# Kernel tuning notes

Measured on AMD Instinct MI355X. Metric: run time of the kernel, lower is better.

## Reference

```python
import jax, jax.numpy as jnp
import numpy as np

TEMPERATURE = 0.07
EPS = 1e-12  # F.normalize eps


def _construct_labels(visual_ids, anchor_idx):
    # Faithful vectorization of the original order-dependent double loop:
    # for i < B-1: final write to labels[i] comes from pair (i, B-1)
    #   -> 1 iff ids[i]==anchor_id and ids[B-1]==anchor_id, else 0
    # for i == B-1: final write comes from pair (B-2, B-1)
    #   -> 1 iff ids[B-1]==anchor_id and ids[B-2]==anchor_id, else 0
    B = visual_ids.shape[0]
    anchor_id = visual_ids[anchor_idx]
    same = visual_ids == anchor_id  # [B] bool
    labels = jnp.where(same & same[B - 1], 1, 0).astype(jnp.int32)
    labels = labels.at[B - 1].set((same[B - 1] & same[B - 2]).astype(jnp.int32))
    return labels


def setup_inputs() -> dict:
    key = jax.random.key(0)
    k1, k2 = jax.random.split(key)
    visual_feat = jax.random.normal(k1, (8192, 512), dtype=jnp.float32)
    visual_ids = jax.random.randint(k2, (8192,), 0, 1024, dtype=jnp.int64 if jax.config.jax_enable_x64 else jnp.int32)
    anchor_idx = 3
    return {"visual_feat": visual_feat, "visual_ids": visual_ids, "anchor_idx": anchor_idx}


def reference(visual_feat, visual_ids, anchor_idx):
    # L2 normalize rows (F.normalize: x / max(||x||, eps))
    norm = jnp.sqrt(jnp.sum(visual_feat * visual_feat, axis=1, keepdims=True))
    f = visual_feat / jnp.maximum(norm, EPS)
    sim = jnp.matmul(f, f.T) / TEMPERATURE  # [B, B]
    labels = _construct_labels(visual_ids, anchor_idx)  # [B] int in {0,1}
    logp = jax.nn.log_softmax(sim, axis=-1)  # [B, B]
    picked = jnp.take_along_axis(logp, labels[:, None], axis=1)[:, 0]
    loss = -jnp.mean(picked)
    return loss
```

## Files before the change

### kernel.cpp

```cpp
#include <hip/hip_runtime.h>


typedef int i32x8 __attribute__((ext_vector_type(8)));
typedef float f32x4 __attribute__((ext_vector_type(4)));

#define B_N 8192
#define D_K 512
#define ROWB 512
#define INVT 14.285714285714286f
#define SCALE_LOG2 20.609929155556622f

static __device__ __forceinline__ void load16_to_lds(const void* g, void* l) {
  __builtin_amdgcn_global_load_lds(
      (const __attribute__((address_space(1))) unsigned int*)g,
      (__attribute__((address_space(3))) unsigned int*)l, 16, 0, 0);
}

__global__ __launch_bounds__(256)
void norm_kernel(const float* __restrict__ x,
                 unsigned char* __restrict__ fQ,
                 float* __restrict__ Z) {
  const int row = blockIdx.x * 4 + (threadIdx.x >> 6);
  const int lane = threadIdx.x & 63;
  const float4* xr = (const float4*)(x + (size_t)row * D_K);
  float4 a = xr[2 * lane];
  float4 b = xr[2 * lane + 1];
  float s = a.x * a.x + a.y * a.y + a.z * a.z + a.w * a.w +
            b.x * b.x + b.y * b.y + b.z * b.z + b.w * b.w;
#pragma unroll
  for (int off = 1; off < 64; off <<= 1) s += __shfl_xor(s, off);
  const float inv = 1.0f / fmaxf(sqrtf(s), 1e-12f);
  int lo = 0, hi = 0;
  lo = __builtin_amdgcn_cvt_pk_fp8_f32(a.x * inv, a.y * inv, lo, false);
  lo = __builtin_amdgcn_cvt_pk_fp8_f32(a.z * inv, a.w * inv, lo, true);
  hi = __builtin_amdgcn_cvt_pk_fp8_f32(b.x * inv, b.y * inv, hi, false);
  hi = __builtin_amdgcn_cvt_pk_fp8_f32(b.z * inv, b.w * inv, hi, true);
  int2 p; p.x = lo; p.y = hi;
  ((int2*)(fQ + (size_t)row * ROWB))[lane] = p;
  if (lane == 0) Z[row] = 0.0f;
}

__global__ __launch_bounds__(256, 2)
void sim_kernel(const unsigned char* __restrict__ fQ,
                float* __restrict__ Z, float* __restrict__ T01,
                float* __restrict__ D) {
  __shared__ unsigned char ldsA[128 * 128];
  __shared__ unsigned char ldsB[128 * 128];

  const int tid = threadIdx.x;
  const int lane = tid & 63;
  const int w = tid >> 6;
  const int wm = w & 1;
  const int wn = w >> 1;
  const int I0 = blockIdx.x * 128;
  const int Jbase = blockIdx.y * 1024;

  const int srow = lane >> 3;
  const int sg = (lane & 7) ^ srow;
  const size_t sOff = (size_t)srow * ROWB + sg * 16;

  const int fr = lane & 15;
  const int q = lane >> 4;
  const int swz = fr & 7;

  const unsigned char* raBase = ldsA + (wm * 64 + fr) * 128;
  const unsigned char* rbBase = ldsB + (wn * 64 + fr) * 128;
  const int off0 = ((2 * q) ^ swz) * 16;
  const int off1 = ((2 * q + 1) ^ swz) * 16;

  float Zp[4][4];
#pragma unroll
  for (int m = 0; m < 4; ++m)
#pragma unroll
    for (int r = 0; r < 4; ++r) Zp[m][r] = 0.0f;

#pragma unroll 1
  for (int jt = 0; jt < 8; ++jt) {
    const int J0 = Jbase + jt * 128;
    f32x4 acc[4][4];
#pragma unroll
    for (int m = 0; m < 4; ++m)
#pragma unroll
      for (int n = 0; n < 4; ++n) acc[m][n] = (f32x4){0.f, 0.f, 0.f, 0.f};

#pragma unroll 1
    for (int kk = 0; kk < 4; ++kk) {
      const int k0 = kk * 128;
      {
        const unsigned char* gA = fQ + (size_t)(I0 + w * 32) * ROWB + k0 + sOff;
        unsigned char* lA = ldsA + (w * 32) * 128;
#pragma unroll
        for (int rr = 0; rr < 32; rr += 8)
          load16_to_lds(gA + (size_t)rr * ROWB, lA + rr * 128);
      }
      {
        const unsigned char* gB = fQ + (size_t)(J0 + w * 32) * ROWB + k0 + sOff;
        unsigned char* lB = ldsB + (w * 32) * 128;
#pragma unroll
        for (int rr = 0; rr < 32; rr += 8)
          load16_to_lds(gB + (size_t)rr * ROWB, lB + rr * 128);
      }
      __syncthreads();

      i32x8 bv[4];
#pragma unroll
      for (int n = 0; n < 4; ++n) {
        const unsigned char* rb = rbBase + n * 16 * 128;
        int4 r0 = *(const int4*)(rb + off0);
        int4 r1 = *(const int4*)(rb + off1);
        bv[n] = (i32x8){r0.x, r0.y, r0.z, r0.w, r1.x, r1.y, r1.z, r1.w};
      }
#pragma unroll
      for (int mh = 0; mh < 2; ++mh) {
        i32x8 av[2];
#pragma unroll
        for (int m = 0; m < 2; ++m) {
          const unsigned char* ra = raBase + (mh * 2 + m) * 16 * 128;
          int4 r0 = *(const int4*)(ra + off0);
          int4 r1 = *(const int4*)(ra + off1);
          av[m] = (i32x8){r0.x, r0.y, r0.z, r0.w, r1.x, r1.y, r1.z, r1.w};
        }
#pragma unroll
        for (int m = 0; m < 2; ++m)
#pragma unroll
          for (int n = 0; n < 4; ++n)
            acc[mh * 2 + m][n] = __builtin_amdgcn_mfma_scale_f32_16x16x128_f8f6f4(
                av[m], bv[n], acc[mh * 2 + m][n], 0, 0, 0, 127, 0, 127);
      }
      __syncthreads();
    }

    if (blockIdx.y == 0 && jt == 0 && wn == 0 && fr < 2) {
#pragma unroll
      for (int m = 0; m < 4; ++m)
#pragma unroll
        for (int r = 0; r < 4; ++r) {
          const int row = I0 + wm * 64 + m * 16 + q * 4 + r;
          T01[row * 2 + fr] = acc[m][0][r] * INVT;
        }
    }

    if (blockIdx.y == (blockIdx.x >> 3) && jt == (blockIdx.x & 7)) {
#pragma unroll
      for (int m = 0; m < 4; ++m)
#pragma unroll
        for (int n = 0; n < 4; ++n) {
          const int col = J0 + wn * 64 + n * 16 + fr;
#pragma unroll
          for (int r = 0; r < 4; ++r) {
            const int row = I0 + wm * 64 + m * 16 + q * 4 + r;
            if (row == col) D[row] = acc[m][n][r];
          }
        }
    }

#pragma unroll
    for (int m = 0; m < 4; ++m)
#pragma unroll
      for (int n = 0; n < 4; ++n)
#pragma unroll
        for (int r = 0; r < 4; ++r)
          Zp[m][r] += exp2f((acc[m][n][r] - 1.0f) * SCALE_LOG2);
  }

#pragma unroll
  for (int m = 0; m < 4; ++m)
#pragma unroll
    for (int r = 0; r < 4; ++r) {
      float v = Zp[m][r];
      v += __shfl_xor(v, 1);
      v += __shfl_xor(v, 2);
      v += __shfl_xor(v, 4);
      v += __shfl_xor(v, 8);
      if (fr == 0) atomicAdd(&Z[I0 + wm * 64 + m * 16 + q * 4 + r], v);
    }
}

__global__ __launch_bounds__(1024)
void finalize_kernel(const float* __restrict__ Z,
                     const float* __restrict__ T01,
                     const float* __restrict__ D,
                     const int* __restrict__ ids,
                     const int* __restrict__ anchor,
                     float* __restrict__ out) {
  __shared__ float red[1024];
  const int t = threadIdx.x;
  const int anchor_id = ids[anchor[0]];
  const int sameLast = (ids[B_N - 1] == anchor_id);
  const int samePrev = (ids[B_N - 2] == anchor_id);
  float sum = 0.0f;
#pragma unroll
  for (int it = 0; it < B_N / 1024; ++it) {
    const int i = it * 1024 + t;
    const int same_i = (ids[i] == anchor_id);
    const int lab = (i < B_N - 1) ? (same_i & sameLast) : (sameLast & samePrev);
    const float tt = T01[i * 2 + lab];
    const float Zc = Z[i] - exp2f((D[i] - 1.0f) * SCALE_LOG2) + 1.0f;
    sum += tt - (INVT + logf(Zc));
  }
  red[t] = sum;
  __syncthreads();
  for (int off = 512; off > 0; off >>= 1) {
    if (t < off) red[t] += red[t + off];
    __syncthreads();
  }
  if (t == 0) out[0] = -red[0] / (float)B_N;
}

extern "C" void kernel_launch(void* const* d_in, const int* in_sizes, int n_in,
                              void* d_out, int out_size, void* d_ws, size_t ws_size,
                              hipStream_t stream) {
  const float* x = (const float*)d_in[0];
  const int* ids = (const int*)d_in[1];
  const int* anchor = (const int*)d_in[2];
  float* out = (float*)d_out;

  unsigned char* fQ = (unsigned char*)d_ws;
  float* Z = (float*)((char*)d_ws + (size_t)B_N * ROWB);
  float* T01 = Z + B_N;
  float* D = T01 + 2 * B_N;

  norm_kernel<<<B_N / 4, 256, 0, stream>>>(x, fQ, Z);
  sim_kernel<<<dim3(64, 8), 256, 0, stream>>>(fQ, Z, T01, D);
  finalize_kernel<<<1, 1024, 0, stream>>>(Z, T01, D, ids, anchor, out);
}
```

Measured before the change: 122.7 us.

## Fuse finalize reduction into sim kernel via last-block atomic counter

Removes the separate finalize kernel launch. Each sim block increments a global counter when it finishes, and the last block to arrive computes the log-softmax loss reduction. Stores to T01 and D become agent-scope atomics so the last block sees them after a threadfence. Launch bounds also change to allow 3 blocks per CU. The cost is a serialized tail: one 256-thread block does all the final work.

```diff
diff --git a/kernel.cpp b/kernel.cpp
--- a/kernel.cpp
+++ b/kernel.cpp
@@ -7,8 +7,12 @@
 #define B_N 8192
 #define D_K 512
 #define ROWB 512
+#define NBLK 512
 #define INVT 14.285714285714286f
 #define SCALE_LOG2 20.609929155556622f
+
+#define AGENT_LOAD(p) __hip_atomic_load((p), __ATOMIC_RELAXED, __HIP_MEMORY_SCOPE_AGENT)
+#define AGENT_STORE(p, v) __hip_atomic_store((p), (v), __ATOMIC_RELAXED, __HIP_MEMORY_SCOPE_AGENT)
 
 static __device__ __forceinline__ void load16_to_lds(const void* g, void* l) {
   __builtin_amdgcn_global_load_lds(
@@ -19,7 +23,8 @@
 __global__ __launch_bounds__(256)
 void norm_kernel(const float* __restrict__ x,
                  unsigned char* __restrict__ fQ,
-                 float* __restrict__ Z) {
+                 float* __restrict__ Z,
+                 unsigned int* __restrict__ cnt) {
   const int row = blockIdx.x * 4 + (threadIdx.x >> 6);
   const int lane = threadIdx.x & 63;
   const float4* xr = (const float4*)(x + (size_t)row * D_K);
@@ -38,22 +43,29 @@
   int2 p; p.x = lo; p.y = hi;
   ((int2*)(fQ + (size_t)row * ROWB))[lane] = p;
   if (lane == 0) Z[row] = 0.0f;
-}
-
-__global__ __launch_bounds__(256, 2)
+  if (blockIdx.x == 0 && threadIdx.x == 0) cnt[0] = 0u;
+}
+
+__global__ __launch_bounds__(256, 3)
 void sim_kernel(const unsigned char* __restrict__ fQ,
                 float* __restrict__ Z, float* __restrict__ T01,
-                float* __restrict__ D) {
+                float* __restrict__ D,
+                const int* __restrict__ ids,
+                const int* __restrict__ anchor,
+                unsigned int* __restrict__ cnt,
+                float* __restrict__ out) {
   __shared__ unsigned char ldsA[128 * 128];
   __shared__ unsigned char ldsB[128 * 128];
+  __shared__ unsigned int s_last;
 
   const int tid = threadIdx.x;
   const int lane = tid & 63;
   const int w = tid >> 6;
   const int wm = w & 1;
   const int wn = w >> 1;
-  const int I0 = blockIdx.x * 128;
-  const int Jbase = blockIdx.y * 1024;
+  const int bx = blockIdx.x, by = blockIdx.y;
+  const int I0 = bx * 128;
+  const int Jbase = by * 1024;
 
   const int srow = lane >> 3;
   const int sg = (lane & 7) ^ srow;
@@ -130,17 +142,17 @@
       __syncthreads();
     }
 
-    if (blockIdx.y == 0 && jt == 0 && wn == 0 && fr < 2) {
+    if (by == 0 && jt == 0 && wn == 0 && fr < 2) {
 #pragma unroll
       for (int m = 0; m < 4; ++m)
 #pragma unroll
         for (int r = 0; r < 4; ++r) {
           const int row = I0 + wm * 64 + m * 16 + q * 4 + r;
-          T01[row * 2 + fr] = acc[m][0][r] * INVT;
+          AGENT_STORE(&T01[row * 2 + fr], acc[m][0][r] * INVT);
         }
     }
 
-    if (blockIdx.y == (blockIdx.x >> 3) && jt == (blockIdx.x & 7)) {
+    if (by == (bx >> 3) && jt == (bx & 7)) {
 #pragma unroll
       for (int m = 0; m < 4; ++m)
 #pragma unroll
@@ -149,7 +161,7 @@
 #pragma unroll
           for (int r = 0; r < 4; ++r) {
             const int row = I0 + wm * 64 + m * 16 + q * 4 + r;
-            if (row == col) D[row] = acc[m][n][r];
+            if (row == col) AGENT_STORE(&D[row], acc[m][n][r]);
           }
         }
     }
@@ -174,37 +186,50 @@
       v += __shfl_xor(v, 8);
       if (fr == 0) atomicAdd(&Z[I0 + wm * 64 + m * 16 + q * 4 + r], v);
     }
-}
-
-__global__ __launch_bounds__(1024)
-void finalize_kernel(const float* __restrict__ Z,
-                     const float* __restrict__ T01,
-                     const float* __restrict__ D,
-                     const int* __restrict__ ids,
-                     const int* __restrict__ anchor,
-                     float* __restrict__ out) {
-  __shared__ float red[1024];
-  const int t = threadIdx.x;
+
+  __syncthreads();
+  __threadfence();
+  if (tid == 0) s_last = atomicAdd(cnt, 1u);
+  __syncthreads();
+  if (s_last != NBLK - 1) return;
+  __threadfence();
+
   const int anchor_id = ids[anchor[0]];
   const int sameLast = (ids[B_N - 1] == anchor_id);
   const int samePrev = (ids[B_N - 2] == anchor_id);
   float sum = 0.0f;
-#pragma unroll
-  for (int it = 0; it < B_N / 1024; ++it) {
-    const int i = it * 1024 + t;
-    const int same_i = (ids[i] == anchor_id);
-    const int lab = (i < B_N - 1) ? (same_i & sameLast) : (sameLast & samePrev);
-    const float tt = T01[i * 2 + lab];
-    const float Zc = Z[i] - exp2f((D[i] - 1.0f) * SCALE_LOG2) + 1.0f;
-    sum += tt - (INVT + logf(Zc));
+#pragma unroll 1
+  for (int ib = 0; ib < 8; ++ib) {
+    int i[4];
+    float z[4], d[4], t0[4], t1[4];
+    int id[4];
+#pragma unroll
+    for (int u = 0; u < 4; ++u) {
+      i[u] = (ib * 4 + u) * 256 + tid;
+      z[u] = AGENT_LOAD(&Z[i[u]]);
+      d[u] = AGENT_LOAD(&D[i[u]]);
+      t0[u] = AGENT_LOAD(&T01[i[u] * 2 + 0]);
+      t1[u] = AGENT_LOAD(&T01[i[u] * 2 + 1]);
+      id[u] = ids[i[u]];
+    }
+#pragma unroll
+    for (int u = 0; u < 4; ++u) {
+      const int same_i = (id[u] == anchor_id);
+      const int lab =
+          (i[u] < B_N - 1) ? (same_i & sameLast) : (sameLast & samePrev);
+      const float tt = lab ? t1[u] : t0[u];
+      const float Zc = z[u] - exp2f((d[u] - 1.0f) * SCALE_LOG2) + 1.0f;
+      sum += tt - (INVT + logf(Zc));
+    }
   }
-  red[t] = sum;
+  float* red = (float*)ldsA;
+  red[tid] = sum;
   __syncthreads();
-  for (int off = 512; off > 0; off >>= 1) {
-    if (t < off) red[t] += red[t + off];
+  for (int off = 128; off > 0; off >>= 1) {
+    if (tid < off) red[tid] += red[tid + off];
     __syncthreads();
   }
-  if (t == 0) out[0] = -red[0] / (float)B_N;
+  if (tid == 0) out[0] = -red[0] / (float)B_N;
 }
 
 extern "C" void kernel_launch(void* const* d_in, const int* in_sizes, int n_in,
@@ -219,8 +244,8 @@
   float* Z = (float*)((char*)d_ws + (size_t)B_N * ROWB);
   float* T01 = Z + B_N;
   float* D = T01 + 2 * B_N;
-
-  norm_kernel<<<B_N / 4, 256, 0, stream>>>(x, fQ, Z);
-  sim_kernel<<<dim3(64, 8), 256, 0, stream>>>(fQ, Z, T01, D);
-  finalize_kernel<<<1, 1024, 0, stream>>>(Z, T01, D, ids, anchor, out);
-}
+  unsigned int* cnt = (unsigned int*)(D + B_N);
+
+  norm_kernel<<<B_N / 4, 256, 0, stream>>>(x, fQ, Z, cnt);
+  sim_kernel<<<dim3(64, 8), 256, 0, stream>>>(fQ, Z, T01, D, ids, anchor, cnt, out);
+}
```

New measurement: 158.9 us. +29.5%, slower.

## Keep the full A row panel resident in LDS across all column tiles

Applied to the files above, without the earlier changes.

The sim kernel now loads the block's 128x512 fp8 A panel into LDS once, across four k-slices, instead of reloading it for every column tile. Only the B tile is streamed in the inner loop, roughly halving per-iteration global-to-LDS traffic. The LDS swizzle and the read offsets are changed to a new k-chunk permutation. The finalize kernel now issues all of its loads up front. The cost is LDS use rising to about 80KB per block, which may limit occupancy.

```diff
diff --git a/kernel.cpp b/kernel.cpp
--- a/kernel.cpp
+++ b/kernel.cpp
@@ -44,7 +44,7 @@
 void sim_kernel(const unsigned char* __restrict__ fQ,
                 float* __restrict__ Z, float* __restrict__ T01,
                 float* __restrict__ D) {
-  __shared__ unsigned char ldsA[128 * 128];
+  __shared__ unsigned char ldsA[4][128 * 128];
   __shared__ unsigned char ldsB[128 * 128];
 
   const int tid = threadIdx.x;
@@ -52,21 +52,33 @@
   const int w = tid >> 6;
   const int wm = w & 1;
   const int wn = w >> 1;
-  const int I0 = blockIdx.x * 128;
-  const int Jbase = blockIdx.y * 1024;
+  const int bx = blockIdx.x, by = blockIdx.y;
+  const int I0 = bx * 128;
+  const int Jbase = by * 1024;
 
   const int srow = lane >> 3;
-  const int sg = (lane & 7) ^ srow;
+  const int sb = lane & 7;
+  const int su = sb ^ srow;
+  const int sg = 2 * (su & 3) + (su >> 2);
   const size_t sOff = (size_t)srow * ROWB + sg * 16;
 
   const int fr = lane & 15;
   const int q = lane >> 4;
   const int swz = fr & 7;
 
-  const unsigned char* raBase = ldsA + (wm * 64 + fr) * 128;
+  const int raRow = (wm * 64 + fr) * 128;
   const unsigned char* rbBase = ldsB + (wn * 64 + fr) * 128;
-  const int off0 = ((2 * q) ^ swz) * 16;
-  const int off1 = ((2 * q + 1) ^ swz) * 16;
+  const int off0 = (q ^ swz) * 16;
+  const int off1 = ((q + 4) ^ swz) * 16;
+
+#pragma unroll
+  for (int kk = 0; kk < 4; ++kk) {
+    const unsigned char* gA = fQ + (size_t)(I0 + w * 32) * ROWB + kk * 128 + sOff;
+    unsigned char* lA = ldsA[kk] + (w * 32) * 128;
+#pragma unroll
+    for (int rr = 0; rr < 32; rr += 8)
+      load16_to_lds(gA + (size_t)rr * ROWB, lA + rr * 128);
+  }
 
   float Zp[4][4];
 #pragma unroll
@@ -87,13 +99,6 @@
     for (int kk = 0; kk < 4; ++kk) {
       const int k0 = kk * 128;
       {
-        const unsigned char* gA = fQ + (size_t)(I0 + w * 32) * ROWB + k0 + sOff;
-        unsigned char* lA = ldsA + (w * 32) * 128;
-#pragma unroll
-        for (int rr = 0; rr < 32; rr += 8)
-          load16_to_lds(gA + (size_t)rr * ROWB, lA + rr * 128);
-      }
-      {
         const unsigned char* gB = fQ + (size_t)(J0 + w * 32) * ROWB + k0 + sOff;
         unsigned char* lB = ldsB + (w * 32) * 128;
 #pragma unroll
@@ -102,6 +107,7 @@
       }
       __syncthreads();
 
+      const unsigned char* raBase = ldsA[kk] + raRow;
       i32x8 bv[4];
 #pragma unroll
       for (int n = 0; n < 4; ++n) {
@@ -130,7 +136,7 @@
       __syncthreads();
     }
 
-    if (blockIdx.y == 0 && jt == 0 && wn == 0 && fr < 2) {
+    if (by == 0 && jt == 0 && wn == 0 && fr < 2) {
 #pragma unroll
       for (int m = 0; m < 4; ++m)
 #pragma unroll
@@ -140,7 +146,7 @@
         }
     }
 
-    if (blockIdx.y == (blockIdx.x >> 3) && jt == (blockIdx.x & 7)) {
+    if (by == (bx >> 3) && jt == (bx & 7)) {
 #pragma unroll
       for (int m = 0; m < 4; ++m)
 #pragma unroll
@@ -188,14 +194,25 @@
   const int anchor_id = ids[anchor[0]];
   const int sameLast = (ids[B_N - 1] == anchor_id);
   const int samePrev = (ids[B_N - 2] == anchor_id);
+  int i[8], id[8];
+  float z[8], d[8], t0[8], t1[8];
+#pragma unroll
+  for (int u = 0; u < 8; ++u) {
+    i[u] = u * 1024 + t;
+    z[u] = Z[i[u]];
+    d[u] = D[i[u]];
+    t0[u] = T01[i[u] * 2 + 0];
+    t1[u] = T01[i[u] * 2 + 1];
+    id[u] = ids[i[u]];
+  }
   float sum = 0.0f;
 #pragma unroll
-  for (int it = 0; it < B_N / 1024; ++it) {
-    const int i = it * 1024 + t;
-    const int same_i = (ids[i] == anchor_id);
-    const int lab = (i < B_N - 1) ? (same_i & sameLast) : (sameLast & samePrev);
-    const float tt = T01[i * 2 + lab];
-    const float Zc = Z[i] - exp2f((D[i] - 1.0f) * SCALE_LOG2) + 1.0f;
+  for (int u = 0; u < 8; ++u) {
+    const int same_i = (id[u] == anchor_id);
+    const int lab =
+        (i[u] < B_N - 1) ? (same_i & sameLast) : (sameLast & samePrev);
+    const float tt = lab ? t1[u] : t0[u];
+    const float Zc = z[u] - exp2f((d[u] - 1.0f) * SCALE_LOG2) + 1.0f;
     sum += tt - (INVT + logf(Zc));
   }
   red[t] = sum;
```

Measured after the change: 118.9 us. 3.1% less time.
